# Kernel optimization log

Measured on AMD Instinct MI355X. Metric: run time of the kernel, lower is better.

Reference implementation:

```python
import jax, jax.numpy as jnp
import numpy as np

NEG_SLOPE = 0.2  # PyG GATConv default LeakyReLU slope


def gat_layer(x, src, dst, W, a_src, a_dst, bias, num_nodes, heads, out_ch, concat):
    # x: [N, in], W: [in, heads*out_ch], a_src/a_dst: [heads, out_ch]
    h = (x @ W).reshape(num_nodes, heads, out_ch)          # [N,H,C]
    alpha_s = jnp.sum(h * a_src, axis=-1)                  # [N,H]
    alpha_d = jnp.sum(h * a_dst, axis=-1)                  # [N,H]
    e = jax.nn.leaky_relu(alpha_s[src] + alpha_d[dst], NEG_SLOPE)  # [E,H]
    # softmax over incoming edges of each destination node
    e_max = jax.ops.segment_max(e, dst, num_segments=num_nodes)   # [N,H]
    e_exp = jnp.exp(e - e_max[dst])                        # [E,H]
    denom = jax.ops.segment_sum(e_exp, dst, num_segments=num_nodes)  # [N,H]
    alpha = e_exp / denom[dst]                             # [E,H]
    msg = h[src] * alpha[:, :, None]                       # [E,H,C]
    out = jax.ops.segment_sum(msg, dst, num_segments=num_nodes)     # [N,H,C]
    if concat:
        out = out.reshape(num_nodes, heads * out_ch)
    else:
        out = out.mean(axis=1)
    return out + bias


def setup_inputs() -> dict:
    key = jax.random.key(0)
    ks = jax.random.split(key, 12)
    N, E = 50000, 800000
    IN, HID, OUT, H = 128, 32, 64, 4
    x = jax.random.normal(ks[0], (N, IN), dtype=jnp.float32)
    edge_index = jax.random.randint(ks[1], (2, E), 0, N, dtype=jnp.int32)
    s = 1.0 / np.sqrt(IN)
    W1 = jax.random.normal(ks[2], (IN, H * HID), dtype=jnp.float32) * s
    a_src1 = jax.random.normal(ks[3], (H, HID), dtype=jnp.float32) * 0.1
    a_dst1 = jax.random.normal(ks[4], (H, HID), dtype=jnp.float32) * 0.1
    b1 = jnp.zeros((H * HID,), dtype=jnp.float32)
    s2 = 1.0 / np.sqrt(H * HID)
    W2 = jax.random.normal(ks[5], (H * HID, OUT), dtype=jnp.float32) * s2
    a_src2 = jax.random.normal(ks[6], (1, OUT), dtype=jnp.float32) * 0.1
    a_dst2 = jax.random.normal(ks[7], (1, OUT), dtype=jnp.float32) * 0.1
    b2 = jnp.zeros((OUT,), dtype=jnp.float32)
    return {"x": x, "edge_index": edge_index, "W1": W1, "a_src1": a_src1,
            "a_dst1": a_dst1, "b1": b1, "W2": W2, "a_src2": a_src2,
            "a_dst2": a_dst2, "b2": b2}


def reference(x, edge_index, W1, a_src1, a_dst1, b1, W2, a_src2, a_dst2, b2):
    N = x.shape[0]
    src, dst = edge_index[0], edge_index[1]
    h = gat_layer(x, src, dst, W1, a_src1, a_dst1, b1, N, heads=4, out_ch=32, concat=True)
    h = jax.nn.elu(h)
    # dropout is identity in eval / p=0.0
    out = gat_layer(h, src, dst, W2, a_src2, a_dst2, b2, N, heads=1, out_ch=64, concat=False)
    return out
```

## Files before the change

kernel.cpp:

```cpp
#include <hip/hip_runtime.h>
#include <hip/hip_bf16.h>

#define C1 128
#define C2 64

typedef __attribute__((ext_vector_type(8))) short short8;
typedef __attribute__((ext_vector_type(4))) float floatx4;

__device__ __forceinline__ float lrelu(float v) { return v > 0.f ? v : 0.2f * v; }

__device__ __forceinline__ unsigned short f2bf(float f) {
    unsigned u = __float_as_uint(f);
    u += 0x7FFFu + ((u >> 16) & 1u);
    return (unsigned short)(u >> 16);
}

__global__ __launch_bounds__(256)
void g1_count_kernel(const float* __restrict__ x, const float* __restrict__ W1,
                     const float* __restrict__ asrc, const float* __restrict__ adst,
                     unsigned short* __restrict__ h1b,
                     float* __restrict__ as1, float* __restrict__ ad1,
                     int N, int nbTile,
                     const int* __restrict__ ei, int* __restrict__ deg, int E) {
    __shared__ __align__(16) unsigned short Bs[128 * 136];
    if (blockIdx.x >= nbTile) {
        const int b = blockIdx.x - nbTile;
        for (int e = b * 256 + threadIdx.x; e < E; e += 1024 * 256) {
            int d = ei[E + e];
            if ((unsigned)d < (unsigned)N) atomicAdd(&deg[d], 1);
        }
        return;
    }
    for (int i = threadIdx.x; i < 128 * 64; i += 256) {
        int col = i & 127;
        int k = (i >> 7) * 2;
        unsigned w0 = f2bf(W1[k * 128 + col]);
        unsigned w1 = f2bf(W1[(k + 1) * 128 + col]);
        *(unsigned*)&Bs[col * 136 + k] = w0 | (w1 << 16);
    }
    __syncthreads();

    const int lane = threadIdx.x & 63, ww = threadIdx.x >> 6;
    const int quad = lane >> 4, l16 = lane & 15;
    const int nodeBase = blockIdx.x * 64 + ww * 16;
    int arow = nodeBase + l16;
    if (arow >= N) arow = N - 1;
    const float* xp = x + (size_t)arow * C1 + quad * 8;
    short8 afr[4];
#pragma unroll
    for (int kk = 0; kk < 4; ++kk) {
        float4 a0 = *(const float4*)(xp + kk * 32);
        float4 a1 = *(const float4*)(xp + kk * 32 + 4);
        short8 fr;
        fr[0] = (short)f2bf(a0.x); fr[1] = (short)f2bf(a0.y);
        fr[2] = (short)f2bf(a0.z); fr[3] = (short)f2bf(a0.w);
        fr[4] = (short)f2bf(a1.x); fr[5] = (short)f2bf(a1.y);
        fr[6] = (short)f2bf(a1.z); fr[7] = (short)f2bf(a1.w);
        afr[kk] = fr;
    }

    float sacc[4], dacc[4];
#pragma unroll
    for (int ct = 0; ct < 8; ++ct) {
        floatx4 acc = {0.f, 0.f, 0.f, 0.f};
        const int col = ct * 16 + l16;
        const unsigned short* bbase = &Bs[col * 136 + quad * 8];
#pragma unroll
        for (int kk = 0; kk < 4; ++kk) {
            short8 bfr = *(const short8*)(bbase + kk * 32);
            acc = __builtin_amdgcn_mfma_f32_16x16x32_bf16(afr[kk], bfr, acc, 0, 0, 0);
        }
#pragma unroll
        for (int reg = 0; reg < 4; ++reg) {
            int node = nodeBase + quad * 4 + reg;
            if (node < N) h1b[(size_t)node * C1 + col] = f2bf(acc[reg]);
        }
        float av = asrc[col];
        float dv = adst[col];
        if ((ct & 1) == 0) {
#pragma unroll
            for (int r = 0; r < 4; ++r) { sacc[r] = 0.f; dacc[r] = 0.f; }
        }
#pragma unroll
        for (int reg = 0; reg < 4; ++reg) {
            float ts = acc[reg] * av;
            float td = acc[reg] * dv;
#pragma unroll
            for (int o = 1; o < 16; o <<= 1) {
                ts += __shfl_xor(ts, o, 64);
                td += __shfl_xor(td, o, 64);
            }
            sacc[reg] += ts;
            dacc[reg] += td;
        }
        if ((ct & 1) == 1 && l16 == 0) {
            int h = ct >> 1;
#pragma unroll
            for (int reg = 0; reg < 4; ++reg) {
                int node = nodeBase + quad * 4 + reg;
                if (node < N) {
                    as1[node * 4 + h] = sacc[reg];
                    ad1[node * 4 + h] = dacc[reg];
                }
            }
        }
    }
}

__global__ __launch_bounds__(1024)
void scanA_kernel(const int* __restrict__ deg, int* __restrict__ offs,
                  int* __restrict__ bsum, int N) {
    __shared__ int wsum[16];
    const int i = blockIdx.x * 1024 + threadIdx.x;
    const int lane = threadIdx.x & 63, wid = threadIdx.x >> 6;
    int v = (i < N) ? deg[i] : 0;
    int x = v;
#pragma unroll
    for (int o = 1; o < 64; o <<= 1) {
        int y = __shfl_up(x, o, 64);
        if (lane >= o) x += y;
    }
    if (lane == 63) wsum[wid] = x;
    __syncthreads();
    if (wid == 0 && lane < 16) {
        int s = wsum[lane];
#pragma unroll
        for (int o = 1; o < 16; o <<= 1) {
            int y = __shfl_up(s, o, 16);
            if (lane >= o) s += y;
        }
        wsum[lane] = s;
    }
    __syncthreads();
    int pre = (wid > 0) ? wsum[wid - 1] : 0;
    int incl = x + pre;
    if (i < N) offs[i] = incl - v;
    if (threadIdx.x == 1023) bsum[blockIdx.x] = incl;
}

__global__ __launch_bounds__(1024)
void scanBC_kernel(int* __restrict__ offs, int* __restrict__ cursor,
                   const int* __restrict__ bsum, int N, int nb) {
    __shared__ int pref;
    const int t = threadIdx.x;
    if (t < 64) {
        int v = (t < nb) ? bsum[t] : 0;
        int x = v;
#pragma unroll
        for (int o = 1; o < 64; o <<= 1) {
            int y = __shfl_up(x, o, 64);
            if (t >= o) x += y;
        }
        if (t == (int)blockIdx.x) pref = x - v;
        if (blockIdx.x == 0 && t == 63) offs[N] = x;
    }
    __syncthreads();
    const int i = blockIdx.x * 1024 + t;
    if (i < N) {
        int o = offs[i] + pref;
        offs[i] = o;
        cursor[i] = o;
    }
}

__global__ __launch_bounds__(256)
void fill_kernel(const int* __restrict__ ei, int* __restrict__ cursor,
                 int* __restrict__ csrc, int N, int E) {
    const int part = blockIdx.x & 7;
    const int bIdx = blockIdx.x >> 3;
    const int bpp  = gridDim.x >> 3;
    const int lo = (int)(((long)N * part) >> 3);
    const int hi = (int)(((long)N * (part + 1)) >> 3);
    for (int e = bIdx * 256 + threadIdx.x; e < E; e += bpp * 256) {
        int d = ei[E + e];
        if (d < lo || d >= hi) continue;
        int s = ei[e];
        if ((unsigned)s >= (unsigned)N) continue;
        int pos = atomicAdd(&cursor[d], 1);
        csrc[pos] = s;
    }
}

__global__ __launch_bounds__(256)
void msg1_csr_kernel(const int* __restrict__ offs, const int* __restrict__ csrc,
                     const unsigned* __restrict__ h1u, const float* __restrict__ as1,
                     const float* __restrict__ ad1, const float* __restrict__ b1,
                     float2* __restrict__ out1, int N) {
    const int d = blockIdx.x * 4 + (threadIdx.x >> 6);
    if (d >= N) return;
    const int lane = threadIdx.x & 63;
    const int beg = offs[d], end = offs[d + 1];
    const int k8 = lane & 7;
    const int whead = (lane >> 3) & 3;
    const int myHead = lane >> 4;
    const float wadh = ad1[d * 4 + whead];
    float accx = 0.f, accy = 0.f, sumw = 0.f;
    for (int jj = beg; jj < end; jj += 8) {
        int idx = jj + k8;
        if (idx >= end) idx = end - 1;
        const int myS = csrc[idx];
        int s[8];
#pragma unroll
        for (int k = 0; k < 8; ++k) s[k] = __shfl(myS, k, 64);
        unsigned rv[8];
#pragma unroll
        for (int k = 0; k < 8; ++k) rv[k] = h1u[(size_t)s[k] * 64 + lane];
        float w = 0.f;
        if (lane < 32 && jj + k8 < end) {
            float a = as1[myS * 4 + whead];
            w = __expf(lrelu(a + wadh));
        }
#pragma unroll
        for (int k = 0; k < 8; ++k) {
            float wk = __shfl(w, myHead * 8 + k, 64);
            sumw += wk;
            accx += wk * __uint_as_float(rv[k] << 16);
            accy += wk * __uint_as_float(rv[k] & 0xFFFF0000u);
        }
    }
    float inv = (sumw > 0.f) ? 1.f / sumw : 0.f;
    float rx = accx * inv + b1[2 * lane];
    float ry = accy * inv + b1[2 * lane + 1];
    rx = rx > 0.f ? rx : expm1f(rx);
    ry = ry > 0.f ? ry : expm1f(ry);
    float2 p; p.x = rx; p.y = ry;
    out1[(size_t)d * 64 + lane] = p;
}

__global__ __launch_bounds__(256)
void gemm2_mfma_kernel(const float* __restrict__ h2, const float* __restrict__ W2,
                       const float* __restrict__ asrc, const float* __restrict__ adst,
                       unsigned short* __restrict__ g2b, float* __restrict__ as2,
                       float* __restrict__ ad2, int N) {
    __shared__ __align__(16) unsigned short Bs[64 * 136];
    for (int i = threadIdx.x; i < 64 * 64; i += 256) {
        int col = i & 63;
        int k = (i >> 6) * 2;
        unsigned w0 = f2bf(W2[k * 64 + col]);
        unsigned w1 = f2bf(W2[(k + 1) * 64 + col]);
        *(unsigned*)&Bs[col * 136 + k] = w0 | (w1 << 16);
    }
    __syncthreads();

    const int lane = threadIdx.x & 63, ww = threadIdx.x >> 6;
    const int quad = lane >> 4, l16 = lane & 15;
    const int nodeBase = blockIdx.x * 64 + ww * 16;
    int arow = nodeBase + l16;
    if (arow >= N) arow = N - 1;
    const float* xp = h2 + (size_t)arow * C1 + quad * 8;
    short8 afr[4];
#pragma unroll
    for (int kk = 0; kk < 4; ++kk) {
        float4 a0 = *(const float4*)(xp + kk * 32);
        float4 a1 = *(const float4*)(xp + kk * 32 + 4);
        short8 fr;
        fr[0] = (short)f2bf(a0.x); fr[1] = (short)f2bf(a0.y);
        fr[2] = (short)f2bf(a0.z); fr[3] = (short)f2bf(a0.w);
        fr[4] = (short)f2bf(a1.x); fr[5] = (short)f2bf(a1.y);
        fr[6] = (short)f2bf(a1.z); fr[7] = (short)f2bf(a1.w);
        afr[kk] = fr;
    }

    float sacc[4] = {0.f,0.f,0.f,0.f}, dacc[4] = {0.f,0.f,0.f,0.f};
#pragma unroll
    for (int ct = 0; ct < 4; ++ct) {
        floatx4 acc = {0.f, 0.f, 0.f, 0.f};
        const int col = ct * 16 + l16;
        const unsigned short* bbase = &Bs[col * 136 + quad * 8];
#pragma unroll
        for (int kk = 0; kk < 4; ++kk) {
            short8 bfr = *(const short8*)(bbase + kk * 32);
            acc = __builtin_amdgcn_mfma_f32_16x16x32_bf16(afr[kk], bfr, acc, 0, 0, 0);
        }
#pragma unroll
        for (int reg = 0; reg < 4; ++reg) {
            int node = nodeBase + quad * 4 + reg;
            if (node < N) g2b[(size_t)node * C2 + col] = f2bf(acc[reg]);
        }
        float av = asrc[col];
        float dv = adst[col];
#pragma unroll
        for (int reg = 0; reg < 4; ++reg) {
            float ts = acc[reg] * av;
            float td = acc[reg] * dv;
#pragma unroll
            for (int o = 1; o < 16; o <<= 1) {
                ts += __shfl_xor(ts, o, 64);
                td += __shfl_xor(td, o, 64);
            }
            sacc[reg] += ts;
            dacc[reg] += td;
        }
    }
    if (l16 == 0) {
#pragma unroll
        for (int reg = 0; reg < 4; ++reg) {
            int node = nodeBase + quad * 4 + reg;
            if (node < N) { as2[node] = sacc[reg]; ad2[node] = dacc[reg]; }
        }
    }
}

__global__ __launch_bounds__(256)
void msg2_csr_kernel(const int* __restrict__ offs, const int* __restrict__ csrc,
                     const unsigned* __restrict__ g2u, const float* __restrict__ as2,
                     const float* __restrict__ ad2, const float* __restrict__ b2,
                     float2* __restrict__ y, int N) {
    const int d = blockIdx.x * 4 + (threadIdx.x >> 6);
    if (d >= N) return;
    const int lane = threadIdx.x & 63;
    const int half = lane >> 5;
    const int l32 = lane & 31;
    const int k16 = lane & 15;
    const int beg = offs[d], end = offs[d + 1];
    const float add = ad2[d];
    float accx = 0.f, accy = 0.f, sumw = 0.f;
    for (int jj = beg; jj < end; jj += 16) {
        int idx = jj + k16;
        if (idx >= end) idx = end - 1;
        const int myS = csrc[idx];
        float w = 0.f;
        if (lane < 16 && jj + k16 < end)
            w = __expf(lrelu(as2[myS] + add));
        int s[8];
#pragma unroll
        for (int k = 0; k < 8; ++k) s[k] = __shfl(myS, 2 * k + half, 64);
        unsigned rv[8];
#pragma unroll
        for (int k = 0; k < 8; ++k) rv[k] = g2u[(size_t)s[k] * 32 + l32];
#pragma unroll
        for (int k = 0; k < 8; ++k) {
            float wk = __shfl(w, 2 * k + half, 64);
            sumw += wk;
            accx += wk * __uint_as_float(rv[k] << 16);
            accy += wk * __uint_as_float(rv[k] & 0xFFFF0000u);
        }
    }
    accx += __shfl_xor(accx, 32, 64);
    accy += __shfl_xor(accy, 32, 64);
    sumw += __shfl_xor(sumw, 32, 64);
    if (half == 0) {
        float inv = (sumw > 0.f) ? 1.f / sumw : 0.f;
        float2 p;
        p.x = accx * inv + b2[2 * l32];
        p.y = accy * inv + b2[2 * l32 + 1];
        y[(size_t)d * 32 + l32] = p;
    }
}

extern "C" void kernel_launch(void* const* d_in, const int* in_sizes, int n_in,
                              void* d_out, int out_size, void* d_ws, size_t ws_size,
                              hipStream_t stream) {
    const float* x    = (const float*)d_in[0];
    const int*   ei   = (const int*)d_in[1];
    const float* W1   = (const float*)d_in[2];
    const float* a_s1 = (const float*)d_in[3];
    const float* a_d1 = (const float*)d_in[4];
    const float* b1   = (const float*)d_in[5];
    const float* W2   = (const float*)d_in[6];
    const float* a_s2 = (const float*)d_in[7];
    const float* a_d2 = (const float*)d_in[8];
    const float* b2   = (const float*)d_in[9];

    const int N = in_sizes[0] / C1;
    const int E = in_sizes[1] / 2;

    auto align16 = [](size_t v) { return (v + 15) & ~(size_t)15; };
    const size_t RF   = 16;
    const size_t ROFF = align16((size_t)(N + 1) * 4);
    const size_t RCUR = align16((size_t)N * 4);
    const size_t RBS  = 256;
    const size_t RSRC = align16((size_t)E * 4);
    const size_t R1   = align16((size_t)N * C1 * 4);
    const size_t R2   = align16((size_t)N * 8 * 4);

    char* base = (char*)d_ws;
    int*  offs   = (int*)(base + RF);
    int*  cursor = (int*)(base + RF + ROFF);
    int*  bsum   = (int*)(base + RF + ROFF + RCUR);
    int*  csrc   = (int*)(base + RF + ROFF + RCUR + RBS);
    char* R1p = base + RF + ROFF + RCUR + RBS + RSRC;
    char* R2p = R1p + R1;
    char* R4p = R2p + R2;
    (void)ws_size;

    unsigned short* h1 = (unsigned short*)R1p;
    unsigned short* g2 = (unsigned short*)R1p;
    float* as1 = (float*)R2p;
    float* ad1 = as1 + (size_t)N * 4;
    float* as2 = (float*)R2p;
    float* ad2 = as2 + N;
    float* out1 = (float*)R4p;

    const int nbScan = (N + 1023) / 1024;
    const int nbTile = (N + 63) / 64;
    const int nbWave4 = (N + 3) / 4;

    hipMemsetAsync(cursor, 0, (size_t)N * 4, stream);
    g1_count_kernel<<<nbTile + 1024, 256, 0, stream>>>(x, W1, a_s1, a_d1,
        h1, as1, ad1, N, nbTile, ei, cursor, E);
    scanA_kernel<<<nbScan, 1024, 0, stream>>>(cursor, offs, bsum, N);
    scanBC_kernel<<<nbScan, 1024, 0, stream>>>(offs, cursor, bsum, N, nbScan);
    fill_kernel<<<1024, 256, 0, stream>>>(ei, cursor, csrc, N, E);
    msg1_csr_kernel<<<nbWave4, 256, 0, stream>>>(offs, csrc, (const unsigned*)h1,
        as1, ad1, b1, (float2*)out1, N);
    gemm2_mfma_kernel<<<nbTile, 256, 0, stream>>>(out1, W2, a_s2, a_d2, g2, as2, ad2, N);
    msg2_csr_kernel<<<nbWave4, 256, 0, stream>>>(offs, csrc, (const unsigned*)g2,
        as2, ad2, b2, (float2*)d_out, N);
}
```

Measured before the change: 255.9 us.

## Partition degree counting by node range and widen gather batches in message kernels

The degree-count blocks now each handle one eighth of the destination range, with eight times as many passes over the edge list. This confines each block's atomics to a smaller, more cache-local slice of the degree array, at the cost of reading the edge indices eight times. Both message-passing kernels now gather twice as many source rows per loop iteration (16 and 32 edges), to increase memory-level parallelism and amortize the index and weight loads. This raises register use, and on short adjacency lists more of the batch is wasted padding.

```diff
diff --git a/kernel.cpp b/kernel.cpp
--- a/kernel.cpp
+++ b/kernel.cpp
@@ -25,9 +25,13 @@
     __shared__ __align__(16) unsigned short Bs[128 * 136];
     if (blockIdx.x >= nbTile) {
         const int b = blockIdx.x - nbTile;
-        for (int e = b * 256 + threadIdx.x; e < E; e += 1024 * 256) {
+        const int part = b & 7;
+        const int bIdx = b >> 3;
+        const int lo = (int)(((long)N * part) >> 3);
+        const int hi = (int)(((long)N * (part + 1)) >> 3);
+        for (int e = bIdx * 256 + threadIdx.x; e < E; e += 128 * 256) {
             int d = ei[E + e];
-            if ((unsigned)d < (unsigned)N) atomicAdd(&deg[d], 1);
+            if (d >= lo && d < hi) atomicAdd(&deg[d], 1);
         }
         return;
     }
@@ -190,29 +194,26 @@
     if (d >= N) return;
     const int lane = threadIdx.x & 63;
     const int beg = offs[d], end = offs[d + 1];
-    const int k8 = lane & 7;
-    const int whead = (lane >> 3) & 3;
-    const int myHead = lane >> 4;
-    const float wadh = ad1[d * 4 + whead];
+    const int e16 = lane & 15;
+    const int head = lane >> 4;
+    const float wadh = ad1[d * 4 + head];
     float accx = 0.f, accy = 0.f, sumw = 0.f;
-    for (int jj = beg; jj < end; jj += 8) {
-        int idx = jj + k8;
+    for (int jj = beg; jj < end; jj += 16) {
+        int idx = jj + e16;
         if (idx >= end) idx = end - 1;
         const int myS = csrc[idx];
-        int s[8];
-#pragma unroll
-        for (int k = 0; k < 8; ++k) s[k] = __shfl(myS, k, 64);
-        unsigned rv[8];
-#pragma unroll
-        for (int k = 0; k < 8; ++k) rv[k] = h1u[(size_t)s[k] * 64 + lane];
         float w = 0.f;
-        if (lane < 32 && jj + k8 < end) {
-            float a = as1[myS * 4 + whead];
-            w = __expf(lrelu(a + wadh));
-        }
-#pragma unroll
-        for (int k = 0; k < 8; ++k) {
-            float wk = __shfl(w, myHead * 8 + k, 64);
+        if (jj + e16 < end)
+            w = __expf(lrelu(as1[myS * 4 + head] + wadh));
+        unsigned rv[16];
+#pragma unroll
+        for (int k = 0; k < 16; ++k) {
+            int s = __shfl(myS, k, 64);
+            rv[k] = h1u[(unsigned)s * 64u + (unsigned)lane];
+        }
+#pragma unroll
+        for (int k = 0; k < 16; ++k) {
+            float wk = __shfl(w, (head << 4) | k, 64);
             sumw += wk;
             accx += wk * __uint_as_float(rv[k] << 16);
             accy += wk * __uint_as_float(rv[k] & 0xFFFF0000u);
@@ -311,25 +312,24 @@
     const int lane = threadIdx.x & 63;
     const int half = lane >> 5;
     const int l32 = lane & 31;
-    const int k16 = lane & 15;
     const int beg = offs[d], end = offs[d + 1];
     const float add = ad2[d];
     float accx = 0.f, accy = 0.f, sumw = 0.f;
-    for (int jj = beg; jj < end; jj += 16) {
-        int idx = jj + k16;
+    for (int jj = beg; jj < end; jj += 32) {
+        int idx = jj + l32;
         if (idx >= end) idx = end - 1;
         const int myS = csrc[idx];
         float w = 0.f;
-        if (lane < 16 && jj + k16 < end)
+        if (lane < 32 && jj + l32 < end)
             w = __expf(lrelu(as2[myS] + add));
-        int s[8];
-#pragma unroll
-        for (int k = 0; k < 8; ++k) s[k] = __shfl(myS, 2 * k + half, 64);
-        unsigned rv[8];
-#pragma unroll
-        for (int k = 0; k < 8; ++k) rv[k] = g2u[(size_t)s[k] * 32 + l32];
-#pragma unroll
-        for (int k = 0; k < 8; ++k) {
+        unsigned rv[16];
+#pragma unroll
+        for (int k = 0; k < 16; ++k) {
+            int s = __shfl(myS, 2 * k + half, 64);
+            rv[k] = g2u[(unsigned)s * 32u + (unsigned)l32];
+        }
+#pragma unroll
+        for (int k = 0; k < 16; ++k) {
             float wk = __shfl(w, 2 * k + half, 64);
             sumw += wk;
             accx += wk * __uint_as_float(rv[k] << 16);
```

New measurement: 256.8 us. No clear change (+0.4%).
